# Optimization experiments

Measured on AMD Instinct MI355X. Metric: run time of the kernel, lower is better.

## Reference

```python
import jax, jax.numpy as jnp
import numpy as np
import math

LEVELS = 256
DISTANCES = [1, 3, 5, 7]
ANGLES_DEG = [0, 45, 90, 135]


def _offsets():
    # offset_row = round(sin(theta)*d), offset_col = round(cos(theta)*d)
    offs = []
    for d in DISTANCES:
        row = []
        for theta in ANGLES_DEG:
            rad = theta * math.pi / 180.0
            orow = int(np.round(np.sin(rad) * d))
            ocol = int(np.round(np.cos(rad) * d))
            row.append((orow, ocol))
        offs.append(row)
    return offs


def _glcm_contrast(q, orow, ocol, rows, cols):
    # q: (H, W) int32 quantized image in [0, LEVELS-1]
    sr = 0 if orow > 0 else -orow
    er = rows - orow if orow > 0 else rows
    sc = 0 if ocol > 0 else -ocol
    ec = cols - ocol if ocol > 0 else cols
    a = q[sr:er, sc:ec]
    b = q[sr + orow:er + orow, sc + ocol:ec + ocol]
    idx = (a * LEVELS + b).ravel()
    # scatter-add co-occurrence histogram (the irregular-access core)
    hist = jnp.zeros((LEVELS * LEVELS,), jnp.float32).at[idx].add(1.0)
    P = hist.reshape(LEVELS, LEVELS)
    P = P + P.T                      # symmetric
    s = P.sum()
    P = P / jnp.where(s == 0, 1.0, s)  # normalize
    lv = jnp.arange(LEVELS, dtype=jnp.float32)
    diff2 = (lv[:, None] - lv[None, :]) ** 2
    return (diff2 * P).sum()         # Haralick contrast


def setup_inputs() -> dict:
    key = jax.random.key(0)
    x = jax.random.normal(key, (32, 1, 1024, 1024), dtype=jnp.float32)
    return {"x": x}


def reference(x):
    B, C, H, W = x.shape
    img = x[:, 0]  # (B, H, W), single channel
    # per-image rescale to [0, LEVELS-1] then truncate to int (matches int() cast)
    mn = img.min(axis=(1, 2), keepdims=True)
    mx = img.max(axis=(1, 2), keepdims=True)
    q = ((LEVELS - 1) * (img - mn) / (mx - mn)).astype(jnp.int32)
    q = jax.lax.stop_gradient(q)
    offs = _offsets()
    rows_out = []
    for d_row in offs:
        cols_out = []
        for (orow, ocol) in d_row:
            f = lambda qi, o=orow, c=ocol: _glcm_contrast(qi, o, c, H, W)
            cols_out.append(jax.vmap(f)(q))  # (B,)
        rows_out.append(jnp.stack(cols_out, axis=-1))  # (B, n_angles)
    out = jnp.stack(rows_out, axis=-2)  # (B, n_dist, n_angles)
    return out[:, None, :, :]  # (B, 1, 4, 4)
```

## Files before the change

### kernel.cpp

```cpp
#include <hip/hip_runtime.h>

#define H 1024
#define W 1024
#define NIMG 32
#define NOFF 16
#define NACC 17
#define TH 64
#define TW 256
#define TROWS 71
#define TSTR 304
#define NTHR 512
#define NWAVE 8
#define NBLK (W / TW * (H / TH) * NIMG)

__device__ __forceinline__ int sdot4i(unsigned a, unsigned b, int c) {
#if __has_builtin(__builtin_amdgcn_sdot4)
    return __builtin_amdgcn_sdot4((int)a, (int)b, c, false);
#else
    c += (int)(signed char)(a)       * (int)(signed char)(b);
    c += (int)(signed char)(a >> 8)  * (int)(signed char)(b >> 8);
    c += (int)(signed char)(a >> 16) * (int)(signed char)(b >> 16);
    c += (int)(signed char)(a >> 24) * (int)(signed char)(b >> 24);
    return c;
#endif
}

__device__ __forceinline__ unsigned funnel(unsigned hi, unsigned lo, int shiftBytes) {
#if __has_builtin(__builtin_amdgcn_alignbit)
    return __builtin_amdgcn_alignbit(hi, lo, shiftBytes * 8);
#else
    unsigned long long pair = (((unsigned long long)hi) << 32) | lo;
    return (unsigned)(pair >> (shiftBytes * 8));
#endif
}

__device__ __forceinline__ int wave_sum(int v) {
    v += __builtin_amdgcn_update_dpp(0, v, 0x111, 0xf, 0xf, false);
    v += __builtin_amdgcn_update_dpp(0, v, 0x112, 0xf, 0xf, false);
    v += __builtin_amdgcn_update_dpp(0, v, 0x114, 0xf, 0xf, false);
    v += __builtin_amdgcn_update_dpp(0, v, 0x118, 0xf, 0xf, false);
    v += __builtin_amdgcn_update_dpp(0, v, 0x142, 0xa, 0xf, false);
    v += __builtin_amdgcn_update_dpp(0, v, 0x143, 0xc, 0xf, false);
    return v;
}

template <int OC>
__device__ __forceinline__ int dot8(const unsigned* w, const unsigned* aw, int acc) {
#pragma unroll
    for (int m = 0; m < 8; ++m) {
        const int S = 16 + 4 * m + OC;
        unsigned b;
        if ((S & 3) == 0) b = w[S >> 2];
        else              b = funnel(w[(S >> 2) + 1], w[S >> 2], S & 3);
        acc = sdot4i(aw[m], b, acc);
    }
    return acc;
}

__device__ __forceinline__ void load16w(const unsigned char* wp, unsigned* w) {
    uint4 t0 = *(const uint4*)(wp);
    uint4 t1 = *(const uint4*)(wp + 16);
    uint4 t2 = *(const uint4*)(wp + 32);
    uint4 t3 = *(const uint4*)(wp + 48);
    w[0] = t0.x;  w[1] = t0.y;  w[2] = t0.z;  w[3] = t0.w;
    w[4] = t1.x;  w[5] = t1.y;  w[6] = t1.z;  w[7] = t1.w;
    w[8] = t2.x;  w[9] = t2.y;  w[10] = t2.z; w[11] = t2.w;
    w[12] = t3.x; w[13] = t3.y; w[14] = t3.z; w[15] = t3.w;
}

__device__ __forceinline__ void load8mid(const unsigned char* wp, unsigned* w) {
    uint4 t1 = *(const uint4*)(wp + 16);
    uint4 t2 = *(const uint4*)(wp + 32);
    w[4] = t1.x;  w[5] = t1.y;  w[6] = t1.z;  w[7] = t1.w;
    w[8] = t2.x;  w[9] = t2.y;  w[10] = t2.z; w[11] = t2.w;
}

__device__ __forceinline__ unsigned pack4(float4 f, float s, float b) {
    unsigned q0 = (unsigned)(int)fmaf(f.x, s, b);
    unsigned q1 = (unsigned)(int)fmaf(f.y, s, b);
    unsigned q2 = (unsigned)(int)fmaf(f.z, s, b);
    unsigned q3 = (unsigned)(int)fmaf(f.w, s, b);
    return (((q0 & 255u)) | ((q1 & 255u) << 8) | ((q2 & 255u) << 16) | ((q3 & 255u) << 24)) ^ 0x80808080u;
}

__global__ __launch_bounds__(256)
void minmax_partial(const float* __restrict__ x, float* __restrict__ pmn,
                    float* __restrict__ pmx, unsigned long long* __restrict__ gacc,
                    int* __restrict__ RowS, int* __restrict__ ColS,
                    unsigned* __restrict__ dctr) {
    int img = blockIdx.y;
    int chunk = blockIdx.x;
    int tid = threadIdx.x;
    if (chunk == 0) {
        if (tid < NACC) gacc[img * NACC + tid] = 0ull;
        if (tid >= 32 && tid < 46) RowS[img * 14 + tid - 32] = 0;
        if (tid >= 64 && tid < 78) ColS[img * 14 + tid - 64] = 0;
        if (img == 0 && tid == 96) *dctr = 0u;
    }
    const float4* b4 = (const float4*)(x + (size_t)img * (H * (size_t)W) +
                                       (size_t)chunk * (H * W / 64));
    float mn = INFINITY, mx = -INFINITY;
    for (int i = tid; i < 4096; i += 256) {
        float4 v = b4[i];
        mn = fminf(mn, fminf(fminf(v.x, v.y), fminf(v.z, v.w)));
        mx = fmaxf(mx, fmaxf(fmaxf(v.x, v.y), fmaxf(v.z, v.w)));
    }
    for (int o = 32; o > 0; o >>= 1) {
        mn = fminf(mn, __shfl_down(mn, o, 64));
        mx = fmaxf(mx, __shfl_down(mx, o, 64));
    }
    __shared__ float smn[4], smx[4];
    int wave = tid >> 6, lane = tid & 63;
    if (lane == 0) { smn[wave] = mn; smx[wave] = mx; }
    __syncthreads();
    if (tid == 0) {
        mn = fminf(fminf(smn[0], smn[1]), fminf(smn[2], smn[3]));
        mx = fmaxf(fmaxf(smx[0], smx[1]), fmaxf(smx[2], smx[3]));
        pmn[img * 64 + chunk] = mn;
        pmx[img * 64 + chunk] = mx;
    }
}

__global__ __launch_bounds__(NTHR)
void glcm_main(const float* __restrict__ x, const float* __restrict__ pmn,
               const float* __restrict__ pmx, unsigned long long* __restrict__ gacc,
               int* __restrict__ RowS, int* __restrict__ ColS,
               int* __restrict__ cornerWS, unsigned* __restrict__ dctr,
               float* __restrict__ out) {
    __shared__ __align__(16) unsigned char tile[TROWS * TSTR];
    __shared__ int wsum[NWAVE][NACC];
    __shared__ int sRB[7], sCB[7];
    __shared__ float sms[2];
    __shared__ int lastFlag;
    int tid = threadIdx.x;
    int img = blockIdx.z;
    int gr0 = blockIdx.y * TH;
    int gc0 = blockIdx.x * TW;

    if (tid < 64) {
        float mn = pmn[img * 64 + tid], mx = pmx[img * 64 + tid];
        for (int o = 32; o > 0; o >>= 1) {
            mn = fminf(mn, __shfl_down(mn, o, 64));
            mx = fmaxf(mx, __shfl_down(mx, o, 64));
        }
        if (tid == 0) {
            float sc = 255.0f / (mx - mn);
            sms[0] = sc; sms[1] = -mn * sc;
        }
    }
    if (tid >= 64 && tid < 71) { sRB[tid - 64] = 0; sCB[tid - 64] = 0; }
    __syncthreads();
    float scale = sms[0], nmb = sms[1];
    const float* xi = x + (size_t)img * (H * (size_t)W);

    for (int slot = tid; slot < TROWS * (TSTR / 16); slot += NTHR) {
        int rr = slot / (TSTR / 16);
        int cc = (slot - rr * (TSTR / 16)) * 16;
        int grow = gr0 + rr;
        int gcol = gc0 - 16 + cc;
        uint4 bytes = make_uint4(0u, 0u, 0u, 0u);
        if (grow < H && gcol >= 0 && gcol < W) {
            const float4* p = (const float4*)(xi + (size_t)grow * W + gcol);
            float4 f0 = p[0], f1 = p[1], f2 = p[2], f3 = p[3];
            bytes.x = pack4(f0, scale, nmb);
            bytes.y = pack4(f1, scale, nmb);
            bytes.z = pack4(f2, scale, nmb);
            bytes.w = pack4(f3, scale, nmb);
        }
        *(uint4*)(tile + rr * TSTR + cc) = bytes;
    }
    __syncthreads();

    int r = tid >> 3;
    int c0 = (tid & 7) * 32;
    const unsigned char* rowp = tile + r * TSTR + 16 + c0;
    const unsigned char* wbase = tile + r * TSTR + c0;

    uint4 av0 = *(const uint4*)(rowp);
    uint4 av1 = *(const uint4*)(rowp + 16);
    unsigned aw[8];
    aw[0] = av0.x; aw[1] = av0.y; aw[2] = av0.z; aw[3] = av0.w;
    aw[4] = av1.x; aw[5] = av1.y; aw[6] = av1.z; aw[7] = av1.w;

    int acc[NACC];
#pragma unroll
    for (int k = 0; k < NACC; ++k) acc[k] = 0;
#pragma unroll
    for (int m = 0; m < 8; ++m) acc[16] = sdot4i(aw[m], aw[m], acc[16]);

    unsigned w[16];
    {
#pragma unroll
        for (int i = 0; i < 8; ++i) w[4 + i] = aw[i];
        uint4 t3 = *(const uint4*)(wbase + 48);
        w[12] = t3.x; w[13] = t3.y; w[14] = t3.z; w[15] = t3.w;
        unsigned f1[9], f3[9];
#pragma unroll
        for (int k = 0; k < 9; ++k) {
            f1[k] = funnel(w[5 + k], w[4 + k], 1);
            f3[k] = funnel(w[5 + k], w[4 + k], 3);
        }
#pragma unroll
        for (int m = 0; m < 8; ++m) {
            acc[0]  = sdot4i(aw[m], f1[m],     acc[0]);
            acc[8]  = sdot4i(aw[m], f1[m + 1], acc[8]);
            acc[4]  = sdot4i(aw[m], f3[m],     acc[4]);
            acc[12] = sdot4i(aw[m], f3[m + 1], acc[12]);
        }
    }
    {
        load16w(wbase + 1 * TSTR, w);
        acc[1] = dot8<1>(w, aw, acc[1]);
        acc[2] = dot8<0>(w, aw, acc[2]);
        acc[3] = dot8<-1>(w, aw, acc[3]);
    }
    {
        load16w(wbase + 2 * TSTR, w);
        unsigned f2[10];
#pragma unroll
        for (int k = 0; k < 10; ++k) f2[k] = funnel(w[4 + k], w[3 + k], 2);
#pragma unroll
        for (int m = 0; m < 8; ++m) {
            acc[5] = sdot4i(aw[m], f2[m + 1], acc[5]);
            acc[7] = sdot4i(aw[m], f2[m],     acc[7]);
        }
    }
    {
        load8mid(wbase + 3 * TSTR, w);
        acc[6] = dot8<0>(w, aw, acc[6]);
    }
    {
        load16w(wbase + 4 * TSTR, w);
        acc[9]  = dot8<4>(w, aw, acc[9]);
        acc[11] = dot8<-4>(w, aw, acc[11]);
    }
    {
        load16w(wbase + 5 * TSTR, w);
        acc[10] = dot8<0>(w, aw, acc[10]);
        acc[13] = dot8<5>(w, aw, acc[13]);
        acc[15] = dot8<-5>(w, aw, acc[15]);
    }
    {
        load8mid(wbase + 7 * TSTR, w);
        acc[14] = dot8<0>(w, aw, acc[14]);
    }

    int wv = tid >> 6, lane = tid & 63;
#pragma unroll
    for (int k = 0; k < NACC; ++k) {
        int t = wave_sum(acc[k]);
        if (lane == 63) wsum[wv][k] = t;
    }

    bool rowTop = (gr0 == 0), rowBot = (gr0 == H - TH);
    bool colLft = (gc0 == 0), colRgt = (gc0 == W - TW);
    if (rowTop || rowBot) {
        int base = rowTop ? 0 : TH - 7;
        for (int idx = tid; idx < 7 * 64; idx += NTHR) {
            int rr = idx >> 6, ww = idx & 63;
            unsigned v = *(const unsigned*)(tile + (base + rr) * TSTR + 16 + 4 * ww);
            atomicAdd(&sRB[rr], sdot4i(v, v, 0));
        }
    }
    if (colLft || colRgt) {
        int cb = colLft ? 16 : 265;
        if (tid < 7 * TH) {
            int rr = tid / 7, j = tid - rr * 7;
            int s = (int)(signed char)tile[rr * TSTR + cb + j];
            atomicAdd(&sCB[j], s * s);
        }
    }
    if (tid < 49) {
        int i = tid / 7, j = tid - i * 7;
        if (rowTop && colLft) {
            int s = (int)(signed char)tile[i * TSTR + 16 + j];
            atomicExch(&cornerWS[(img * 4 + 0) * 49 + tid], s * s);
        }
        if (rowTop && colRgt) {
            int s = (int)(signed char)tile[i * TSTR + 271 - j];
            atomicExch(&cornerWS[(img * 4 + 1) * 49 + tid], s * s);
        }
        if (rowBot && colLft) {
            int s = (int)(signed char)tile[(TH - 1 - i) * TSTR + 16 + j];
            atomicExch(&cornerWS[(img * 4 + 2) * 49 + tid], s * s);
        }
        if (rowBot && colRgt) {
            int s = (int)(signed char)tile[(TH - 1 - i) * TSTR + 271 - j];
            atomicExch(&cornerWS[(img * 4 + 3) * 49 + tid], s * s);
        }
    }
    __syncthreads();
    if (tid < NACC) {
        int s = 0;
#pragma unroll
        for (int w8 = 0; w8 < NWAVE; ++w8) s += wsum[w8][tid];
        atomicAdd(&gacc[img * NACC + tid], (unsigned long long)(long long)s);
    }
    if (tid < 7) {
        if (rowTop) atomicAdd(&RowS[img * 14 + tid], sRB[tid]);
        if (rowBot) atomicAdd(&RowS[img * 14 + 7 + tid], sRB[tid]);
        if (colLft) atomicAdd(&ColS[img * 14 + tid], sCB[tid]);
        if (colRgt) atomicAdd(&ColS[img * 14 + 7 + tid], sCB[tid]);
    }

    __syncthreads();
    if (tid == 0) {
        unsigned prev = atomicAdd(dctr, 1u);
        lastFlag = (prev == (unsigned)(NBLK - 1)) ? 1 : 0;
    }
    __syncthreads();
    if (lastFlag) {
        const int ORO[16] = {0,1,1,1, 0,2,3,2, 0,4,5,4, 0,5,7,5};
        const int OCO[16] = {1,1,0,-1, 3,2,0,-2, 5,4,0,-4, 7,5,0,-5};
        int oimg = tid >> 4, k = tid & 15;
        int orr = ORO[k], oc = OCO[k], aoc = oc < 0 ? -oc : oc;
        long long RT = 0, RB = 0, CL = 0, CR = 0;
        for (int i = 0; i < orr; ++i) {
            RT += __hip_atomic_load(&RowS[oimg * 14 + i],
                                    __ATOMIC_RELAXED, __HIP_MEMORY_SCOPE_AGENT);
            RB += __hip_atomic_load(&RowS[oimg * 14 + 13 - i],
                                    __ATOMIC_RELAXED, __HIP_MEMORY_SCOPE_AGENT);
        }
        for (int i = 0; i < aoc; ++i) {
            CL += __hip_atomic_load(&ColS[oimg * 14 + i],
                                    __ATOMIC_RELAXED, __HIP_MEMORY_SCOPE_AGENT);
            CR += __hip_atomic_load(&ColS[oimg * 14 + 13 - i],
                                    __ATOMIC_RELAXED, __HIP_MEMORY_SCOPE_AGENT);
        }
        long long CA = oc > 0 ? CR : CL;
        long long CB = oc > 0 ? CL : CR;
        const int* crA = cornerWS + (oimg * 4 + (oc >= 0 ? 3 : 2)) * 49;
        const int* crB = cornerWS + (oimg * 4 + (oc >= 0 ? 0 : 1)) * 49;
        long long PSa = 0, PSb = 0;
        for (int i = 0; i < orr; ++i)
            for (int j = 0; j < aoc; ++j) {
                PSa += __hip_atomic_load(&crA[i * 7 + j],
                                         __ATOMIC_RELAXED, __HIP_MEMORY_SCOPE_AGENT);
                PSb += __hip_atomic_load(&crB[i * 7 + j],
                                         __ATOMIC_RELAXED, __HIP_MEMORY_SCOPE_AGENT);
            }
        long long corr = -(RT + RB + CA + CB) + PSa + PSb;
        long long cross = (long long)__hip_atomic_load(&gacc[oimg * NACC + k],
                                    __ATOMIC_RELAXED, __HIP_MEMORY_SCOPE_AGENT);
        long long tsum  = (long long)__hip_atomic_load(&gacc[oimg * NACC + 16],
                                    __ATOMIC_RELAXED, __HIP_MEMORY_SCOPE_AGENT);
        long long num = 2 * tsum + corr - 2 * cross;
        double n = (double)(H - orr) * (double)(W - aoc);
        out[tid] = (float)((double)num / n);
    }
}

extern "C" void kernel_launch(void* const* d_in, const int* in_sizes, int n_in,
                              void* d_out, int out_size, void* d_ws, size_t ws_size,
                              hipStream_t stream) {
    const float* x = (const float*)d_in[0];
    float* out = (float*)d_out;
    char* ws = (char*)d_ws;
    float* pmn = (float*)ws;
    float* pmx = (float*)(ws + 8192);
    unsigned long long* gacc = (unsigned long long*)(ws + 16384);
    int* RowS = (int*)(ws + 20736);
    int* ColS = (int*)(ws + 22528);
    int* cornerWS = (int*)(ws + 24320);
    unsigned* dctr = (unsigned*)(ws + 49408);

    minmax_partial<<<dim3(64, NIMG), 256, 0, stream>>>(x, pmn, pmx, gacc, RowS,
                                                       ColS, dctr);
    glcm_main<<<dim3(W / TW, H / TH, NIMG), NTHR, 0, stream>>>(x, pmn, pmx, gacc,
                                                               RowS, ColS, cornerWS,
                                                               dctr, out);
}
```

Baseline: 243.4 us.

## Shorten wave reductions via LDS staging and use per-image completion counters

Replaces the full 64-lane DPP wave reduction of 17 accumulators with a 4-lane DPP reduction, stages per-group partials in a larger shared array, and finishes the sum across 136 threads with an 8-lane DPP step. It also replaces the single global completion counter with one counter per image, so the last block of each image writes that image's 16 outputs instead of one final block computing all 512. This is meant to cut DPP instruction count and serialized tail work, at the cost of more shared memory (about 8.7KB extra) and more LDS traffic.

Result: faster. 234.9 us (-3.5%).

```diff
diff --git a/kernel.cpp b/kernel.cpp
--- a/kernel.cpp
+++ b/kernel.cpp
@@ -11,7 +11,7 @@
 #define TSTR 304
 #define NTHR 512
 #define NWAVE 8
-#define NBLK (W / TW * (H / TH) * NIMG)
+#define IBLK (W / TW * (H / TH))
 
 __device__ __forceinline__ int sdot4i(unsigned a, unsigned b, int c) {
 #if __has_builtin(__builtin_amdgcn_sdot4)
@@ -34,13 +34,15 @@
 #endif
 }
 
-__device__ __forceinline__ int wave_sum(int v) {
-    v += __builtin_amdgcn_update_dpp(0, v, 0x111, 0xf, 0xf, false);
-    v += __builtin_amdgcn_update_dpp(0, v, 0x112, 0xf, 0xf, false);
-    v += __builtin_amdgcn_update_dpp(0, v, 0x114, 0xf, 0xf, false);
-    v += __builtin_amdgcn_update_dpp(0, v, 0x118, 0xf, 0xf, false);
-    v += __builtin_amdgcn_update_dpp(0, v, 0x142, 0xa, 0xf, false);
-    v += __builtin_amdgcn_update_dpp(0, v, 0x143, 0xc, 0xf, false);
+__device__ __forceinline__ int group4_sum(int v) {
+    v += __builtin_amdgcn_update_dpp(0, v, 0xB1, 0xf, 0xf, false);
+    v += __builtin_amdgcn_update_dpp(0, v, 0x4E, 0xf, 0xf, false);
+    return v;
+}
+
+__device__ __forceinline__ int group8_sum(int v) {
+    v = group4_sum(v);
+    v += __builtin_amdgcn_update_dpp(0, v, 0x141, 0xf, 0xf, false);
     return v;
 }
 
@@ -95,7 +97,7 @@
         if (tid < NACC) gacc[img * NACC + tid] = 0ull;
         if (tid >= 32 && tid < 46) RowS[img * 14 + tid - 32] = 0;
         if (tid >= 64 && tid < 78) ColS[img * 14 + tid - 64] = 0;
-        if (img == 0 && tid == 96) *dctr = 0u;
+        if (tid == 96) dctr[img] = 0u;
     }
     const float4* b4 = (const float4*)(x + (size_t)img * (H * (size_t)W) +
                                        (size_t)chunk * (H * W / 64));
@@ -128,7 +130,7 @@
                int* __restrict__ cornerWS, unsigned* __restrict__ dctr,
                float* __restrict__ out) {
     __shared__ __align__(16) unsigned char tile[TROWS * TSTR];
-    __shared__ int wsum[NWAVE][NACC];
+    __shared__ int wsum2[NWAVE][16][NACC];
     __shared__ int sRB[7], sCB[7];
     __shared__ float sms[2];
     __shared__ int lastFlag;
@@ -246,10 +248,13 @@
     }
 
     int wv = tid >> 6, lane = tid & 63;
-#pragma unroll
-    for (int k = 0; k < NACC; ++k) {
-        int t = wave_sum(acc[k]);
-        if (lane == 63) wsum[wv][k] = t;
+    int t[NACC];
+#pragma unroll
+    for (int k = 0; k < NACC; ++k) t[k] = group4_sum(acc[k]);
+    if ((lane & 3) == 0) {
+        int g = lane >> 2;
+#pragma unroll
+        for (int k = 0; k < NACC; ++k) wsum2[wv][g][k] = t[k];
     }
 
     bool rowTop = (gr0 == 0), rowBot = (gr0 == H - TH);
@@ -290,11 +295,14 @@
         }
     }
     __syncthreads();
-    if (tid < NACC) {
+    if (tid < NACC * 8) {
+        int k = tid >> 3, wvv = tid & 7;
         int s = 0;
 #pragma unroll
-        for (int w8 = 0; w8 < NWAVE; ++w8) s += wsum[w8][tid];
-        atomicAdd(&gacc[img * NACC + tid], (unsigned long long)(long long)s);
+        for (int g = 0; g < 16; ++g) s += wsum2[wvv][g][k];
+        s = group8_sum(s);
+        if (wvv == 0)
+            atomicAdd(&gacc[img * NACC + k], (unsigned long long)(long long)s);
     }
     if (tid < 7) {
         if (rowTop) atomicAdd(&RowS[img * 14 + tid], sRB[tid]);
@@ -305,32 +313,32 @@
 
     __syncthreads();
     if (tid == 0) {
-        unsigned prev = atomicAdd(dctr, 1u);
-        lastFlag = (prev == (unsigned)(NBLK - 1)) ? 1 : 0;
-    }
-    __syncthreads();
-    if (lastFlag) {
+        unsigned prev = atomicAdd(&dctr[img], 1u);
+        lastFlag = (prev == (unsigned)(IBLK - 1)) ? 1 : 0;
+    }
+    __syncthreads();
+    if (lastFlag && tid < NOFF) {
         const int ORO[16] = {0,1,1,1, 0,2,3,2, 0,4,5,4, 0,5,7,5};
         const int OCO[16] = {1,1,0,-1, 3,2,0,-2, 5,4,0,-4, 7,5,0,-5};
-        int oimg = tid >> 4, k = tid & 15;
+        int k = tid;
         int orr = ORO[k], oc = OCO[k], aoc = oc < 0 ? -oc : oc;
         long long RT = 0, RB = 0, CL = 0, CR = 0;
         for (int i = 0; i < orr; ++i) {
-            RT += __hip_atomic_load(&RowS[oimg * 14 + i],
-                                    __ATOMIC_RELAXED, __HIP_MEMORY_SCOPE_AGENT);
-            RB += __hip_atomic_load(&RowS[oimg * 14 + 13 - i],
+            RT += __hip_atomic_load(&RowS[img * 14 + i],
+                                    __ATOMIC_RELAXED, __HIP_MEMORY_SCOPE_AGENT);
+            RB += __hip_atomic_load(&RowS[img * 14 + 13 - i],
                                     __ATOMIC_RELAXED, __HIP_MEMORY_SCOPE_AGENT);
         }
         for (int i = 0; i < aoc; ++i) {
-            CL += __hip_atomic_load(&ColS[oimg * 14 + i],
-                                    __ATOMIC_RELAXED, __HIP_MEMORY_SCOPE_AGENT);
-            CR += __hip_atomic_load(&ColS[oimg * 14 + 13 - i],
+            CL += __hip_atomic_load(&ColS[img * 14 + i],
+                                    __ATOMIC_RELAXED, __HIP_MEMORY_SCOPE_AGENT);
+            CR += __hip_atomic_load(&ColS[img * 14 + 13 - i],
                                     __ATOMIC_RELAXED, __HIP_MEMORY_SCOPE_AGENT);
         }
         long long CA = oc > 0 ? CR : CL;
         long long CB = oc > 0 ? CL : CR;
-        const int* crA = cornerWS + (oimg * 4 + (oc >= 0 ? 3 : 2)) * 49;
-        const int* crB = cornerWS + (oimg * 4 + (oc >= 0 ? 0 : 1)) * 49;
+        const int* crA = cornerWS + (img * 4 + (oc >= 0 ? 3 : 2)) * 49;
+        const int* crB = cornerWS + (img * 4 + (oc >= 0 ? 0 : 1)) * 49;
         long long PSa = 0, PSb = 0;
         for (int i = 0; i < orr; ++i)
             for (int j = 0; j < aoc; ++j) {
@@ -340,13 +348,13 @@
                                          __ATOMIC_RELAXED, __HIP_MEMORY_SCOPE_AGENT);
             }
         long long corr = -(RT + RB + CA + CB) + PSa + PSb;
-        long long cross = (long long)__hip_atomic_load(&gacc[oimg * NACC + k],
-                                    __ATOMIC_RELAXED, __HIP_MEMORY_SCOPE_AGENT);
-        long long tsum  = (long long)__hip_atomic_load(&gacc[oimg * NACC + 16],
+        long long cross = (long long)__hip_atomic_load(&gacc[img * NACC + k],
+                                    __ATOMIC_RELAXED, __HIP_MEMORY_SCOPE_AGENT);
+        long long tsum  = (long long)__hip_atomic_load(&gacc[img * NACC + 16],
                                     __ATOMIC_RELAXED, __HIP_MEMORY_SCOPE_AGENT);
         long long num = 2 * tsum + corr - 2 * cross;
         double n = (double)(H - orr) * (double)(W - aoc);
-        out[tid] = (float)((double)num / n);
+        out[img * NOFF + k] = (float)((double)num / n);
     }
 }
 
```
